# Kernel tuning notes

Hardware: AMD Instinct MI355X
Metric: run time of the kernel (lower is better)

Reference implementation:

```python
import jax, jax.numpy as jnp
import numpy as np

N_NODES = 50000
N_EDGES = 800000
IN_DIM = 128
HIDDEN = 32
NHEAD = 4
OUT_DIM = 64
NEG_SLOPE = 0.2


def setup_inputs() -> dict:
    key = jax.random.key(0)
    ks = jax.random.split(key, 8)
    x = jax.random.normal(ks[0], (N_NODES, IN_DIM), dtype=jnp.float32)
    edge_index = jax.random.randint(ks[1], (2, N_EDGES), 0, N_NODES, dtype=jnp.int64)
    # layer 1: fc (in_dim -> nhead*hidden), attn [nhead, 2*hidden]
    W1 = jax.random.normal(ks[2], (IN_DIM, NHEAD * HIDDEN), dtype=jnp.float32) * 0.1
    attn1 = jax.random.normal(ks[3], (NHEAD, 2 * HIDDEN), dtype=jnp.float32) * 0.1
    # layer 2: fc (nhead*hidden -> 1*out_dim), attn [1, 2*out_dim]
    W2 = jax.random.normal(ks[4], (NHEAD * HIDDEN, OUT_DIM), dtype=jnp.float32) * 0.1
    attn2 = jax.random.normal(ks[5], (1, 2 * OUT_DIM), dtype=jnp.float32) * 0.1
    # extra output head: Linear(out_dim, out_dim) with bias
    head_W = jax.random.normal(ks[6], (OUT_DIM, OUT_DIM), dtype=jnp.float32) * 0.1
    head_b = jax.random.normal(ks[7], (OUT_DIM,), dtype=jnp.float32) * 0.1
    return {"x": x, "edge_index": edge_index, "W1": W1, "attn1": attn1,
            "W2": W2, "attn2": attn2, "head_W": head_W, "head_b": head_b}


def _gat_layer(x, W, attn, row, col, num_nodes, heads):
    """One GATConv: linear proj, edge attention, segment softmax over dst (col), scatter-add."""
    f_out = W.shape[1] // heads
    h = (x @ W).reshape(num_nodes, heads, f_out)            # [N, H, F]
    a_l, a_r = attn[:, :f_out], attn[:, f_out:]              # split attn for src/dst parts
    e_src = jnp.einsum('nhf,hf->nh', h, a_l)                 # [N, H]
    e_dst = jnp.einsum('nhf,hf->nh', h, a_r)                 # [N, H]
    alpha = e_src[row] + e_dst[col]                          # [E, H] == cat(h[row],h[col])·attn
    alpha = jax.nn.leaky_relu(alpha, NEG_SLOPE)
    # segment softmax grouped by destination node (col); self-loops guarantee non-empty segs
    amax = jax.ops.segment_max(alpha, col, num_segments=num_nodes)
    ex = jnp.exp(alpha - amax[col])
    denom = jax.ops.segment_sum(ex, col, num_segments=num_nodes)
    a = ex / denom[col]                                      # [E, H]
    msg = h[row] * a[:, :, None]                             # [E, H, F]
    out = jax.ops.segment_sum(msg, col, num_segments=num_nodes)  # [N, H, F]
    return out.reshape(num_nodes, heads * f_out)


def reference(x, edge_index, W1, attn1, W2, attn2, head_W, head_b):
    n = x.shape[0]
    loops = jnp.arange(n, dtype=edge_index.dtype)
    row = jnp.concatenate([edge_index[0], loops])
    col = jnp.concatenate([edge_index[1], loops])
    h = _gat_layer(x, W1, attn1, row, col, n, NHEAD)         # [N, NHEAD*HIDDEN]
    h = jax.nn.relu(h)                                       # intermediate-layer activation
    h = _gat_layer(h, W2, attn2, row, col, n, 1)             # [N, OUT_DIM] (last: no act)
    out = h @ head_W + head_b                                # extra_output_fc head
    return out
```

## Files before the change

kernel.cpp:

```cpp
#include <hip/hip_runtime.h>
#include <math.h>

#define N_NODES 50000
#define E_RAW 800000
#define E_TOT 850000
#define NEG_SLOPE 0.2f
#define G1_BLOCKS ((N_NODES + 63) / 64)
#define NBUCK 391
#define EPB 2048
#define PBLK ((E_TOT + EPB - 1) / EPB)

typedef __attribute__((ext_vector_type(8))) short bf16x8;
typedef __attribute__((ext_vector_type(4))) float f32x4;

__device__ __forceinline__ float lrelu(float a) { return a > 0.f ? a : NEG_SLOPE * a; }

__device__ __forceinline__ unsigned f2bf(float f) {
    unsigned u = __float_as_uint(f);
    return (u + 0x7fff + ((u >> 16) & 1)) >> 16;
}
__device__ __forceinline__ unsigned pack2(float a, float b) {
    return f2bf(a) | (f2bf(b) << 16);
}
__device__ __forceinline__ float bflo(unsigned p) { return __uint_as_float(p << 16); }
__device__ __forceinline__ float bfhi(unsigned p) { return __uint_as_float(p & 0xffff0000u); }

__global__ void k_prep(const float* __restrict__ W1, const float* __restrict__ W2,
                       unsigned* __restrict__ Btg, unsigned* __restrict__ B2tg) {
    int c = blockIdx.x;
    int tq = threadIdx.x;
    if (c < 128) {
        Btg[c * 64 + tq] = pack2(W1[(2 * tq) * 128 + c], W1[(2 * tq + 1) * 128 + c]);
    } else {
        int c2 = c - 128;
        B2tg[c2 * 64 + tq] = pack2(W2[(2 * tq) * 64 + c2], W2[(2 * tq + 1) * 64 + c2]);
    }
}

__global__ void k_gemm1_p1(const float* __restrict__ A, const unsigned* __restrict__ Btg,
                           const float* __restrict__ aux, uint2* __restrict__ C,
                           float* __restrict__ es, float* __restrict__ ed,
                           const int* __restrict__ ei, int* __restrict__ hist2d) {
    __shared__ unsigned As[64 * 64];
    if (blockIdx.x >= G1_BLOCKS) {
        int blk = blockIdx.x - G1_BLOCKS;
        int* h = (int*)As;
        for (int i = threadIdx.x; i < NBUCK; i += 256) h[i] = 0;
        __syncthreads();
        int base = blk * EPB;
        for (int i = threadIdx.x; i < EPB; i += 256) {
            int e = base + i;
            if (e >= E_TOT) break;
            int col = (e < E_RAW) ? ei[E_RAW + e] : (e - E_RAW);
            atomicAdd(&h[col >> 7], 1);
        }
        __syncthreads();
        for (int i = threadIdx.x; i < NBUCK; i += 256) hist2d[i * PBLK + blk] = h[i];
        return;
    }
    int t = threadIdx.x;
    int m0 = blockIdx.x * 64;
    int rows = min(64, N_NODES - m0);
    const float4* A4 = (const float4*)(A + (size_t)m0 * 128);
    for (int i = t; i < rows * 32; i += 256) {
        int row = i >> 5, k4 = i & 31;
        float4 v = A4[i];
        int byte = (k4 * 8) ^ ((row & 7) << 4);
        unsigned* p = &As[row * 64 + (byte >> 2)];
        p[0] = pack2(v.x, v.y);
        p[1] = pack2(v.z, v.w);
    }
    __syncthreads();
    int lane = t & 63, wave = t >> 6;
    int r15 = lane & 15, g = lane >> 4;
    int arow = wave * 16 + r15;
    f32x4 acc[8];
#pragma unroll
    for (int i = 0; i < 8; ++i) acc[i] = (f32x4){0.f, 0.f, 0.f, 0.f};
    const char* Abase = (const char*)As + arow * 256;
    int swz = (arow & 7) << 4;
    const char* Bbase = (const char*)Btg;
#pragma unroll
    for (int s = 0; s < 4; ++s) {
        bf16x8 xf = *(const bf16x8*)(Abase + ((64 * s + 16 * g) ^ swz));
#pragma unroll
        for (int tt = 0; tt < 8; ++tt) {
            bf16x8 wf = *(const bf16x8*)(Bbase + ((16 * tt + r15) * 256 + 64 * s + 16 * g));
            acc[tt] = __builtin_amdgcn_mfma_f32_16x16x32_bf16(wf, xf, acc[tt], 0, 0, 0);
        }
    }
    int grow = m0 + arow;
    bool valid = (arow < rows);
    if (valid) {
        uint2* C2 = C + (size_t)grow * 32;
#pragma unroll
        for (int tt = 0; tt < 8; ++tt) {
            uint2 v; v.x = pack2(acc[tt][0], acc[tt][1]); v.y = pack2(acc[tt][2], acc[tt][3]);
            C2[4 * tt + g] = v;
        }
    }
    float ps0 = 0.f, ps1 = 0.f, ps2 = 0.f, ps3 = 0.f;
    float pd0 = 0.f, pd1 = 0.f, pd2 = 0.f, pd3 = 0.f;
#pragma unroll
    for (int tt = 0; tt < 8; ++tt) {
        int h = tt >> 1;
        int fin = 16 * (tt & 1) + 4 * g;
        float4 alv = *(const float4*)(aux + h * 64 + fin);
        float4 arv = *(const float4*)(aux + h * 64 + 32 + fin);
        float s4 = acc[tt][0] * alv.x + acc[tt][1] * alv.y + acc[tt][2] * alv.z + acc[tt][3] * alv.w;
        float d4 = acc[tt][0] * arv.x + acc[tt][1] * arv.y + acc[tt][2] * arv.z + acc[tt][3] * arv.w;
        if (h == 0) { ps0 += s4; pd0 += d4; }
        else if (h == 1) { ps1 += s4; pd1 += d4; }
        else if (h == 2) { ps2 += s4; pd2 += d4; }
        else { ps3 += s4; pd3 += d4; }
    }
#pragma unroll
    for (int mask = 16; mask <= 32; mask <<= 1) {
        ps0 += __shfl_xor(ps0, mask); ps1 += __shfl_xor(ps1, mask);
        ps2 += __shfl_xor(ps2, mask); ps3 += __shfl_xor(ps3, mask);
        pd0 += __shfl_xor(pd0, mask); pd1 += __shfl_xor(pd1, mask);
        pd2 += __shfl_xor(pd2, mask); pd3 += __shfl_xor(pd3, mask);
    }
    if (valid) {
        float psg = (g == 0) ? ps0 : (g == 1) ? ps1 : (g == 2) ? ps2 : ps3;
        float pdg = (g == 0) ? pd0 : (g == 1) ? pd1 : (g == 2) ? pd2 : pd3;
        es[grow * 4 + g] = psg;
        ed[grow * 4 + g] = pdg;
    }
}

__global__ void k_p2a(const int* __restrict__ hist2d, int* __restrict__ off2d,
                      int* __restrict__ bucktot) {
    __shared__ int sh[512];
    int b = blockIdx.x, t = threadIdx.x;
    int v = (t < PBLK) ? hist2d[b * PBLK + t] : 0;
    sh[t] = v;
    __syncthreads();
    for (int ofs = 1; ofs < 512; ofs <<= 1) {
        int u = (t >= ofs) ? sh[t - ofs] : 0;
        __syncthreads();
        sh[t] += u;
        __syncthreads();
    }
    if (t < PBLK) off2d[b * PBLK + t] = sh[t] - v;
    if (t == 511) bucktot[b] = sh[511];
}

__global__ void k_p2b(const int* __restrict__ bucktot, int* __restrict__ bucketbase) {
    __shared__ int sh[512];
    int t = threadIdx.x;
    int v = (t < NBUCK) ? bucktot[t] : 0;
    sh[t] = v;
    __syncthreads();
    for (int ofs = 1; ofs < 512; ofs <<= 1) {
        int u = (t >= ofs) ? sh[t - ofs] : 0;
        __syncthreads();
        sh[t] += u;
        __syncthreads();
    }
    if (t < NBUCK) bucketbase[t] = sh[t] - v;
    if (t == 511) bucketbase[NBUCK] = sh[511];
}

__global__ void k_p3(const int* __restrict__ ei, const int* __restrict__ off2d,
                     const int* __restrict__ bucketbase, unsigned* __restrict__ part) {
    __shared__ int h[NBUCK];
    __shared__ int basebuf[NBUCK];
    int blk = blockIdx.x, t = threadIdx.x;
    for (int i = t; i < NBUCK; i += 256) {
        h[i] = 0;
        basebuf[i] = bucketbase[i] + off2d[i * PBLK + blk];
    }
    __syncthreads();
    int base = blk * EPB;
    for (int i = t; i < EPB; i += 256) {
        int e = base + i;
        if (e >= E_TOT) break;
        int col, src;
        if (e < E_RAW) { col = ei[E_RAW + e]; src = ei[e]; }
        else { col = src = e - E_RAW; }
        int b = col >> 7;
        int lr = atomicAdd(&h[b], 1);
        part[basebuf[b] + lr] = (unsigned)src | ((unsigned)(col & 127) << 16);
    }
}

__global__ void k_p4(const unsigned* __restrict__ part, const int* __restrict__ bucketbase,
                     int* __restrict__ off, unsigned short* __restrict__ srcs) {
    __shared__ int h[128];
    __shared__ int colofs[128];
    int b = blockIdx.x, t = threadIdx.x;
    int s0 = bucketbase[b], s1 = bucketbase[b + 1];
    if (t < 128) h[t] = 0;
    __syncthreads();
    for (int i = s0 + t; i < s1; i += 256) atomicAdd(&h[part[i] >> 16], 1);
    __syncthreads();
    if (t == 0) {
        int acc = 0;
        for (int c = 0; c < 128; ++c) { colofs[c] = acc; acc += h[c]; }
    }
    __syncthreads();
    int colbase = b * 128, ncols = min(128, N_NODES - colbase);
    if (t < ncols) off[colbase + t] = s0 + colofs[t];
    if (b == NBUCK - 1 && t == 0) off[N_NODES] = s1;
    if (t < 128) h[t] = colofs[t];
    __syncthreads();
    for (int i = s0 + t; i < s1; i += 256) {
        unsigned u = part[i];
        int c = u >> 16;
        int slot = atomicAdd(&h[c], 1);
        srcs[s0 + slot] = (unsigned short)(u & 0xffffu);
    }
}

__global__ void k_gemm2m(const unsigned* __restrict__ A, const unsigned* __restrict__ B2tg,
                         const float* __restrict__ aux, uint2* __restrict__ C,
                         float* __restrict__ es, float* __restrict__ ed) {
    __shared__ unsigned As[64 * 64];
    int t = threadIdx.x;
    int m0 = blockIdx.x * 64;
    int rows = min(64, N_NODES - m0);
    const uint4* A4 = (const uint4*)(A + (size_t)m0 * 64);
    for (int i = t; i < rows * 16; i += 256) {
        int row = i >> 4, q = i & 15;
        uint4 v = A4[i];
        int byte = (q * 16) ^ ((row & 7) << 4);
        unsigned* p = &As[row * 64 + (byte >> 2)];
        p[0] = v.x; p[1] = v.y; p[2] = v.z; p[3] = v.w;
    }
    __syncthreads();
    int lane = t & 63, wave = t >> 6;
    int r15 = lane & 15, g = lane >> 4;
    int arow = wave * 16 + r15;
    f32x4 acc[4];
#pragma unroll
    for (int i = 0; i < 4; ++i) acc[i] = (f32x4){0.f, 0.f, 0.f, 0.f};
    const char* Abase = (const char*)As + arow * 256;
    int swz = (arow & 7) << 4;
    const char* Bbase = (const char*)B2tg;
#pragma unroll
    for (int s = 0; s < 4; ++s) {
        bf16x8 xf = *(const bf16x8*)(Abase + ((64 * s + 16 * g) ^ swz));
#pragma unroll
        for (int tt = 0; tt < 4; ++tt) {
            bf16x8 wf = *(const bf16x8*)(Bbase + ((16 * tt + r15) * 256 + 64 * s + 16 * g));
            acc[tt] = __builtin_amdgcn_mfma_f32_16x16x32_bf16(wf, xf, acc[tt], 0, 0, 0);
        }
    }
    int grow = m0 + arow;
    bool valid = (arow < rows);
    if (valid) {
        uint2* C2 = C + (size_t)grow * 16;
#pragma unroll
        for (int tt = 0; tt < 4; ++tt) {
            uint2 v; v.x = pack2(acc[tt][0], acc[tt][1]); v.y = pack2(acc[tt][2], acc[tt][3]);
            C2[4 * tt + g] = v;
        }
    }
    float pl = 0.f, pr = 0.f;
#pragma unroll
    for (int tt = 0; tt < 4; ++tt) {
        int f0 = 16 * tt + 4 * g;
        float4 alv = *(const float4*)(aux + f0);
        float4 arv = *(const float4*)(aux + 64 + f0);
        pl += acc[tt][0] * alv.x + acc[tt][1] * alv.y + acc[tt][2] * alv.z + acc[tt][3] * alv.w;
        pr += acc[tt][0] * arv.x + acc[tt][1] * arv.y + acc[tt][2] * arv.z + acc[tt][3] * arv.w;
    }
#pragma unroll
    for (int mask = 16; mask <= 32; mask <<= 1) {
        pl += __shfl_xor(pl, mask);
        pr += __shfl_xor(pr, mask);
    }
    if (valid && g == 0) { es[grow] = pl; ed[grow] = pr; }
}

__global__ void k_head(const float* __restrict__ A, const float* __restrict__ B,
                       const float* __restrict__ aux, float* __restrict__ Cv) {
    constexpr int K = 64, MT = 32;
    __shared__ float As[MT * K];
    int m0 = blockIdx.x * MT;
    int t = threadIdx.x, g = t >> 4, l = t & 15;
    int rows = min(MT, N_NODES - m0);
    const float4* A4 = (const float4*)(A + (size_t)m0 * K);
    float4* S4 = (float4*)As;
    for (int i = t; i < rows * (K / 4); i += 64) S4[i] = A4[i];
    __syncthreads();
    float acc[8][4];
#pragma unroll
    for (int r = 0; r < 8; ++r)
#pragma unroll
        for (int c = 0; c < 4; ++c) acc[r][c] = 0.f;
    const float4* B4 = (const float4*)B;
    for (int kk = 0; kk < K / 4; ++kk) {
        float4 b0 = B4[(4 * kk + 0) * 16 + l];
        float4 b1 = B4[(4 * kk + 1) * 16 + l];
        float4 b2 = B4[(4 * kk + 2) * 16 + l];
        float4 b3 = B4[(4 * kk + 3) * 16 + l];
#pragma unroll
        for (int r = 0; r < 8; ++r) {
            float4 a = ((const float4*)(As + (g * 8 + r) * K))[kk];
            acc[r][0] = fmaf(a.x, b0.x, fmaf(a.y, b1.x, fmaf(a.z, b2.x, fmaf(a.w, b3.x, acc[r][0]))));
            acc[r][1] = fmaf(a.x, b0.y, fmaf(a.y, b1.y, fmaf(a.z, b2.y, fmaf(a.w, b3.y, acc[r][1]))));
            acc[r][2] = fmaf(a.x, b0.z, fmaf(a.y, b1.z, fmaf(a.z, b2.z, fmaf(a.w, b3.z, acc[r][2]))));
            acc[r][3] = fmaf(a.x, b0.w, fmaf(a.y, b1.w, fmaf(a.z, b2.w, fmaf(a.w, b3.w, acc[r][3]))));
        }
    }
    float4* C = (float4*)Cv;
    float4 bv = ((const float4*)aux)[l];
#pragma unroll
    for (int r = 0; r < 8; ++r) {
        int row = m0 + g * 8 + r;
        if (row < N_NODES) {
            float4 v;
            v.x = acc[r][0] + bv.x; v.y = acc[r][1] + bv.y;
            v.z = acc[r][2] + bv.z; v.w = acc[r][3] + bv.w;
            C[(size_t)row * 16 + l] = v;
        }
    }
}

__global__ void k_agg1(const unsigned* __restrict__ h1b, const float* __restrict__ es,
                       const float* __restrict__ ed, const int* __restrict__ off,
                       const unsigned short* __restrict__ srcs, unsigned* __restrict__ out1) {
    int n = blockIdx.x * (blockDim.x >> 6) + (threadIdx.x >> 6);
    int lane = threadIdx.x & 63;
    if (n >= N_NODES) return;
    int myh = lane & 3;
    int jj = lane >> 2;
    float edh = ed[n * 4 + myh];
    int s = off[n], e = off[n + 1];
    int l16 = lane & 15;
    int esub = lane >> 4;
    int hcL = l16 >> 2;
    float acc[8];
#pragma unroll
    for (int i = 0; i < 8; ++i) acc[i] = 0.f;
    float psum = 0.f;
    for (int base = s; base < e; base += 16) {
        int cnt = e - base;
        int srcj = 0;
        float w = 0.f;
        if (jj < cnt) {
            srcj = srcs[base + jj];
            w = __expf(lrelu(es[srcj * 4 + myh] + edh));
        }
        psum += w;
        for (int j2 = 0; j2 < 16 && j2 < cnt; j2 += 4) {
            int eidx = j2 + esub;
            int src = __shfl(srcj, eidx * 4);
            float wv = __shfl(w, eidx * 4 + hcL);
            uint4 pv = *((const uint4*)(h1b + (size_t)src * 64 + l16 * 4));
            acc[0] = fmaf(bflo(pv.x), wv, acc[0]);
            acc[1] = fmaf(bfhi(pv.x), wv, acc[1]);
            acc[2] = fmaf(bflo(pv.y), wv, acc[2]);
            acc[3] = fmaf(bfhi(pv.y), wv, acc[3]);
            acc[4] = fmaf(bflo(pv.z), wv, acc[4]);
            acc[5] = fmaf(bfhi(pv.z), wv, acc[5]);
            acc[6] = fmaf(bflo(pv.w), wv, acc[6]);
            acc[7] = fmaf(bfhi(pv.w), wv, acc[7]);
        }
    }
#pragma unroll
    for (int mask = 4; mask <= 32; mask <<= 1) psum += __shfl_xor(psum, mask);
    float inv = 1.f / __shfl(psum, hcL);
#pragma unroll
    for (int i = 0; i < 8; ++i) {
        acc[i] += __shfl_xor(acc[i], 16);
        acc[i] += __shfl_xor(acc[i], 32);
    }
    if (esub == 0) {
        uint4 o;
        o.x = pack2(fmaxf(acc[0] * inv, 0.f), fmaxf(acc[1] * inv, 0.f));
        o.y = pack2(fmaxf(acc[2] * inv, 0.f), fmaxf(acc[3] * inv, 0.f));
        o.z = pack2(fmaxf(acc[4] * inv, 0.f), fmaxf(acc[5] * inv, 0.f));
        o.w = pack2(fmaxf(acc[6] * inv, 0.f), fmaxf(acc[7] * inv, 0.f));
        *((uint4*)(out1 + (size_t)n * 64 + l16 * 4)) = o;
    }
}

__global__ void k_agg2(const unsigned* __restrict__ h2b, const float* __restrict__ es,
                       const float* __restrict__ ed, const int* __restrict__ off,
                       const unsigned short* __restrict__ srcs, float* __restrict__ outv) {
    int n = blockIdx.x * (blockDim.x >> 6) + (threadIdx.x >> 6);
    int lane = threadIdx.x & 63;
    if (n >= N_NODES) return;
    float edv = ed[n];
    int s = off[n], e = off[n + 1];
    int l16 = lane & 15;
    int esub = lane >> 4;
    const uint2* gp = (const uint2*)h2b;
    float a0 = 0.f, a1 = 0.f, a2 = 0.f, a3 = 0.f, psum = 0.f;
    for (int base = s; base < e; base += 16) {
        int cnt = e - base;
        int srcj = 0;
        float w = 0.f;
        if (lane < 16 && lane < cnt) {
            srcj = srcs[base + lane];
            w = __expf(lrelu(es[srcj] + edv));
        }
        psum += w;
        for (int j2 = 0; j2 < 16 && j2 < cnt; j2 += 4) {
            int eidx = j2 + esub;
            int src = __shfl(srcj, eidx);
            float wv = __shfl(w, eidx);
            uint2 pv = gp[(size_t)src * 16 + l16];
            a0 = fmaf(bflo(pv.x), wv, a0);
            a1 = fmaf(bfhi(pv.x), wv, a1);
            a2 = fmaf(bflo(pv.y), wv, a2);
            a3 = fmaf(bfhi(pv.y), wv, a3);
        }
    }
#pragma unroll
    for (int mask = 1; mask <= 8; mask <<= 1) psum += __shfl_xor(psum, mask);
    float inv = 1.f / __shfl(psum, 0);
    a0 += __shfl_xor(a0, 16); a0 += __shfl_xor(a0, 32);
    a1 += __shfl_xor(a1, 16); a1 += __shfl_xor(a1, 32);
    a2 += __shfl_xor(a2, 16); a2 += __shfl_xor(a2, 32);
    a3 += __shfl_xor(a3, 16); a3 += __shfl_xor(a3, 32);
    if (esub == 0) {
        float4 o;
        o.x = a0 * inv; o.y = a1 * inv; o.z = a2 * inv; o.w = a3 * inv;
        ((float4*)outv)[(size_t)n * 16 + l16] = o;
    }
}

extern "C" void kernel_launch(void* const* d_in, const int* in_sizes, int n_in,
                              void* d_out, int out_size, void* d_ws, size_t ws_size,
                              hipStream_t stream) {
    const float* x     = (const float*)d_in[0];
    const int*   ei    = (const int*)d_in[1];
    const float* W1    = (const float*)d_in[2];
    const float* attn1 = (const float*)d_in[3];
    const float* W2    = (const float*)d_in[4];
    const float* attn2 = (const float*)d_in[5];
    const float* headW = (const float*)d_in[6];
    const float* headb = (const float*)d_in[7];
    float* out = (float*)d_out;

    char* ws = (char*)d_ws;
    size_t o = 0;
    auto alloc = [&](size_t bytes) -> void* {
        o = (o + 255) & ~(size_t)255;
        void* p = ws + o;
        o += bytes;
        return p;
    };
    unsigned*       h1b    = (unsigned*)alloc((size_t)N_NODES * 128 * 2);
    unsigned*       out1b  = (unsigned*)alloc((size_t)N_NODES * 128 * 2);
    unsigned*       h2b    = (unsigned*)alloc((size_t)N_NODES * 64 * 2);
    float*          h2agg  = (float*)alloc((size_t)N_NODES * 64 * 4);
    float*          e1s    = (float*)alloc((size_t)N_NODES * 4 * 4);
    float*          e1d    = (float*)alloc((size_t)N_NODES * 4 * 4);
    float*          e2s    = (float*)alloc((size_t)N_NODES * 4);
    float*          e2d    = (float*)alloc((size_t)N_NODES * 4);
    int*            off    = (int*)alloc((size_t)(N_NODES + 1) * 4);
    unsigned short* srcs   = (unsigned short*)alloc((size_t)E_TOT * 2);
    unsigned*       Btg    = (unsigned*)alloc((size_t)128 * 64 * 4);
    unsigned*       B2tg   = (unsigned*)alloc((size_t)64 * 64 * 4);
    int*            hist2d = (int*)alloc((size_t)NBUCK * PBLK * 4);
    int*            off2d  = (int*)alloc((size_t)NBUCK * PBLK * 4);
    int*            bucktot = (int*)alloc((size_t)NBUCK * 4);
    int*            bucketbase = (int*)alloc((size_t)(NBUCK + 1) * 4);
    unsigned*       part   = (unsigned*)alloc((size_t)E_TOT * 4);

    k_prep<<<192, 64, 0, stream>>>(W1, W2, Btg, B2tg);

    k_gemm1_p1<<<G1_BLOCKS + PBLK, 256, 0, stream>>>(
        x, Btg, attn1, (uint2*)h1b, e1s, e1d, ei, hist2d);

    k_p2a<<<NBUCK, 512, 0, stream>>>(hist2d, off2d, bucktot);
    k_p2b<<<1, 512, 0, stream>>>(bucktot, bucketbase);
    k_p3<<<PBLK, 256, 0, stream>>>(ei, off2d, bucketbase, part);
    k_p4<<<NBUCK, 256, 0, stream>>>(part, bucketbase, off, srcs);

    k_agg1<<<N_NODES / 4, 256, 0, stream>>>(h1b, e1s, e1d, off, srcs, out1b);

    k_gemm2m<<<(N_NODES + 63) / 64, 256, 0, stream>>>(out1b, B2tg, attn2, (uint2*)h2b, e2s, e2d);
    k_agg2<<<N_NODES / 4, 256, 0, stream>>>(h2b, e2s, e2d, off, srcs, h2agg);

    k_head<<<(N_NODES + 31) / 32, 64, 0, stream>>>(h2agg, headW, headb, out);
}
```

Baseline: 229.8 us.

## Fold bucket scan into partition kernels, fuse head into agg2, batch gather loads

Removes the single-block bucket-base scan kernel by having each partition block recompute the prefix scan of bucket totals redundantly, which also raises those kernels to 512 threads. Fuses the output linear head into the layer-2 aggregation kernel, staging head weights in shared memory so the fp32 intermediate is never written to or re-read from global memory. Restructures both aggregation inner loops to issue four gather loads before consuming them, increasing memory-level parallelism. The trade-offs are redundant scan work per block, a 16KB weight load per aggregation block, and removal of the early-exit and the partial-edge-group guard in the gather loops.

After: 219.5 us. 4.5% less time.

```diff
diff --git a/kernel.cpp b/kernel.cpp
--- a/kernel.cpp
+++ b/kernel.cpp
@@ -146,34 +146,26 @@
     if (t == 511) bucktot[b] = sh[511];
 }
 
-__global__ void k_p2b(const int* __restrict__ bucktot, int* __restrict__ bucketbase) {
+__global__ void k_p3(const int* __restrict__ ei, const int* __restrict__ off2d,
+                     const int* __restrict__ bucktot, unsigned* __restrict__ part) {
     __shared__ int sh[512];
-    int t = threadIdx.x;
-    int v = (t < NBUCK) ? bucktot[t] : 0;
-    sh[t] = v;
-    __syncthreads();
-    for (int ofs = 1; ofs < 512; ofs <<= 1) {
-        int u = (t >= ofs) ? sh[t - ofs] : 0;
-        __syncthreads();
-        sh[t] += u;
-        __syncthreads();
-    }
-    if (t < NBUCK) bucketbase[t] = sh[t] - v;
-    if (t == 511) bucketbase[NBUCK] = sh[511];
-}
-
-__global__ void k_p3(const int* __restrict__ ei, const int* __restrict__ off2d,
-                     const int* __restrict__ bucketbase, unsigned* __restrict__ part) {
     __shared__ int h[NBUCK];
     __shared__ int basebuf[NBUCK];
     int blk = blockIdx.x, t = threadIdx.x;
-    for (int i = t; i < NBUCK; i += 256) {
-        h[i] = 0;
-        basebuf[i] = bucketbase[i] + off2d[i * PBLK + blk];
-    }
+    int v = (t < NBUCK) ? bucktot[t] : 0;
+    sh[t] = v;
+    if (t < NBUCK) h[t] = 0;
+    __syncthreads();
+    for (int ofs = 1; ofs < 512; ofs <<= 1) {
+        int u = (t >= ofs) ? sh[t - ofs] : 0;
+        __syncthreads();
+        sh[t] += u;
+        __syncthreads();
+    }
+    if (t < NBUCK) basebuf[t] = (sh[t] - v) + off2d[t * PBLK + blk];
     __syncthreads();
     int base = blk * EPB;
-    for (int i = t; i < EPB; i += 256) {
+    for (int i = t; i < EPB; i += 512) {
         int e = base + i;
         if (e >= E_TOT) break;
         int col, src;
@@ -185,15 +177,27 @@
     }
 }
 
-__global__ void k_p4(const unsigned* __restrict__ part, const int* __restrict__ bucketbase,
+__global__ void k_p4(const unsigned* __restrict__ part, const int* __restrict__ bucktot,
                      int* __restrict__ off, unsigned short* __restrict__ srcs) {
+    __shared__ int sh[512];
     __shared__ int h[128];
     __shared__ int colofs[128];
+    __shared__ int s0sh, s1sh;
     int b = blockIdx.x, t = threadIdx.x;
-    int s0 = bucketbase[b], s1 = bucketbase[b + 1];
+    int v = (t < NBUCK) ? bucktot[t] : 0;
+    sh[t] = v;
     if (t < 128) h[t] = 0;
     __syncthreads();
-    for (int i = s0 + t; i < s1; i += 256) atomicAdd(&h[part[i] >> 16], 1);
+    for (int ofs = 1; ofs < 512; ofs <<= 1) {
+        int u = (t >= ofs) ? sh[t - ofs] : 0;
+        __syncthreads();
+        sh[t] += u;
+        __syncthreads();
+    }
+    if (t == 0) { s1sh = sh[b]; s0sh = sh[b] - bucktot[b]; }
+    __syncthreads();
+    int s0 = s0sh, s1 = s1sh;
+    for (int i = s0 + t; i < s1; i += 512) atomicAdd(&h[part[i] >> 16], 1);
     __syncthreads();
     if (t == 0) {
         int acc = 0;
@@ -205,7 +209,7 @@
     if (b == NBUCK - 1 && t == 0) off[N_NODES] = s1;
     if (t < 128) h[t] = colofs[t];
     __syncthreads();
-    for (int i = s0 + t; i < s1; i += 256) {
+    for (int i = s0 + t; i < s1; i += 512) {
         unsigned u = part[i];
         int c = u >> 16;
         int slot = atomicAdd(&h[c], 1);
@@ -274,51 +278,6 @@
     if (valid && g == 0) { es[grow] = pl; ed[grow] = pr; }
 }
 
-__global__ void k_head(const float* __restrict__ A, const float* __restrict__ B,
-                       const float* __restrict__ aux, float* __restrict__ Cv) {
-    constexpr int K = 64, MT = 32;
-    __shared__ float As[MT * K];
-    int m0 = blockIdx.x * MT;
-    int t = threadIdx.x, g = t >> 4, l = t & 15;
-    int rows = min(MT, N_NODES - m0);
-    const float4* A4 = (const float4*)(A + (size_t)m0 * K);
-    float4* S4 = (float4*)As;
-    for (int i = t; i < rows * (K / 4); i += 64) S4[i] = A4[i];
-    __syncthreads();
-    float acc[8][4];
-#pragma unroll
-    for (int r = 0; r < 8; ++r)
-#pragma unroll
-        for (int c = 0; c < 4; ++c) acc[r][c] = 0.f;
-    const float4* B4 = (const float4*)B;
-    for (int kk = 0; kk < K / 4; ++kk) {
-        float4 b0 = B4[(4 * kk + 0) * 16 + l];
-        float4 b1 = B4[(4 * kk + 1) * 16 + l];
-        float4 b2 = B4[(4 * kk + 2) * 16 + l];
-        float4 b3 = B4[(4 * kk + 3) * 16 + l];
-#pragma unroll
-        for (int r = 0; r < 8; ++r) {
-            float4 a = ((const float4*)(As + (g * 8 + r) * K))[kk];
-            acc[r][0] = fmaf(a.x, b0.x, fmaf(a.y, b1.x, fmaf(a.z, b2.x, fmaf(a.w, b3.x, acc[r][0]))));
-            acc[r][1] = fmaf(a.x, b0.y, fmaf(a.y, b1.y, fmaf(a.z, b2.y, fmaf(a.w, b3.y, acc[r][1]))));
-            acc[r][2] = fmaf(a.x, b0.z, fmaf(a.y, b1.z, fmaf(a.z, b2.z, fmaf(a.w, b3.z, acc[r][2]))));
-            acc[r][3] = fmaf(a.x, b0.w, fmaf(a.y, b1.w, fmaf(a.z, b2.w, fmaf(a.w, b3.w, acc[r][3]))));
-        }
-    }
-    float4* C = (float4*)Cv;
-    float4 bv = ((const float4*)aux)[l];
-#pragma unroll
-    for (int r = 0; r < 8; ++r) {
-        int row = m0 + g * 8 + r;
-        if (row < N_NODES) {
-            float4 v;
-            v.x = acc[r][0] + bv.x; v.y = acc[r][1] + bv.y;
-            v.z = acc[r][2] + bv.z; v.w = acc[r][3] + bv.w;
-            C[(size_t)row * 16 + l] = v;
-        }
-    }
-}
-
 __global__ void k_agg1(const unsigned* __restrict__ h1b, const float* __restrict__ es,
                        const float* __restrict__ ed, const int* __restrict__ off,
                        const unsigned short* __restrict__ srcs, unsigned* __restrict__ out1) {
@@ -345,19 +304,29 @@
             w = __expf(lrelu(es[srcj * 4 + myh] + edh));
         }
         psum += w;
-        for (int j2 = 0; j2 < 16 && j2 < cnt; j2 += 4) {
-            int eidx = j2 + esub;
-            int src = __shfl(srcj, eidx * 4);
-            float wv = __shfl(w, eidx * 4 + hcL);
-            uint4 pv = *((const uint4*)(h1b + (size_t)src * 64 + l16 * 4));
-            acc[0] = fmaf(bflo(pv.x), wv, acc[0]);
-            acc[1] = fmaf(bfhi(pv.x), wv, acc[1]);
-            acc[2] = fmaf(bflo(pv.y), wv, acc[2]);
-            acc[3] = fmaf(bfhi(pv.y), wv, acc[3]);
-            acc[4] = fmaf(bflo(pv.z), wv, acc[4]);
-            acc[5] = fmaf(bfhi(pv.z), wv, acc[5]);
-            acc[6] = fmaf(bflo(pv.w), wv, acc[6]);
-            acc[7] = fmaf(bfhi(pv.w), wv, acc[7]);
+        int src4[4];
+        float wv4[4];
+#pragma unroll
+        for (int q = 0; q < 4; ++q) {
+            int eidx = 4 * q + esub;
+            src4[q] = __shfl(srcj, eidx * 4);
+            wv4[q] = __shfl(w, eidx * 4 + hcL);
+        }
+        uint4 pv4[4];
+#pragma unroll
+        for (int q = 0; q < 4; ++q)
+            pv4[q] = *((const uint4*)(h1b + (size_t)src4[q] * 64 + l16 * 4));
+#pragma unroll
+        for (int q = 0; q < 4; ++q) {
+            float wv = wv4[q];
+            acc[0] = fmaf(bflo(pv4[q].x), wv, acc[0]);
+            acc[1] = fmaf(bfhi(pv4[q].x), wv, acc[1]);
+            acc[2] = fmaf(bflo(pv4[q].y), wv, acc[2]);
+            acc[3] = fmaf(bfhi(pv4[q].y), wv, acc[3]);
+            acc[4] = fmaf(bflo(pv4[q].z), wv, acc[4]);
+            acc[5] = fmaf(bfhi(pv4[q].z), wv, acc[5]);
+            acc[6] = fmaf(bflo(pv4[q].w), wv, acc[6]);
+            acc[7] = fmaf(bfhi(pv4[q].w), wv, acc[7]);
         }
     }
 #pragma unroll
@@ -378,12 +347,22 @@
     }
 }
 
-__global__ void k_agg2(const unsigned* __restrict__ h2b, const float* __restrict__ es,
-                       const float* __restrict__ ed, const int* __restrict__ off,
-                       const unsigned short* __restrict__ srcs, float* __restrict__ outv) {
-    int n = blockIdx.x * (blockDim.x >> 6) + (threadIdx.x >> 6);
-    int lane = threadIdx.x & 63;
-    if (n >= N_NODES) return;
+__global__ void k_agg2h(const unsigned* __restrict__ h2b, const float* __restrict__ es,
+                        const float* __restrict__ ed, const int* __restrict__ off,
+                        const unsigned short* __restrict__ srcs,
+                        const float* __restrict__ headW, const float* __restrict__ headb,
+                        float* __restrict__ outv) {
+    __shared__ float Wsh[64 * 64];
+    __shared__ float rowsh[4][64];
+    int t = threadIdx.x;
+    {
+        const float4* W4 = (const float4*)headW;
+        float4* S4 = (float4*)Wsh;
+        for (int i = t; i < 1024; i += 256) S4[i] = W4[i];
+    }
+    int wavei = t >> 6;
+    int n = blockIdx.x * 4 + wavei;
+    int lane = t & 63;
     float edv = ed[n];
     int s = off[n], e = off[n + 1];
     int l16 = lane & 15;
@@ -399,15 +378,23 @@
             w = __expf(lrelu(es[srcj] + edv));
         }
         psum += w;
-        for (int j2 = 0; j2 < 16 && j2 < cnt; j2 += 4) {
-            int eidx = j2 + esub;
-            int src = __shfl(srcj, eidx);
-            float wv = __shfl(w, eidx);
-            uint2 pv = gp[(size_t)src * 16 + l16];
-            a0 = fmaf(bflo(pv.x), wv, a0);
-            a1 = fmaf(bfhi(pv.x), wv, a1);
-            a2 = fmaf(bflo(pv.y), wv, a2);
-            a3 = fmaf(bfhi(pv.y), wv, a3);
+        int src4[4];
+        float wv4[4];
+#pragma unroll
+        for (int q = 0; q < 4; ++q) {
+            int eidx = 4 * q + esub;
+            src4[q] = __shfl(srcj, eidx);
+            wv4[q] = __shfl(w, eidx);
+        }
+        uint2 pv4[4];
+#pragma unroll
+        for (int q = 0; q < 4; ++q) pv4[q] = gp[(size_t)src4[q] * 16 + l16];
+#pragma unroll
+        for (int q = 0; q < 4; ++q) {
+            a0 = fmaf(bflo(pv4[q].x), wv4[q], a0);
+            a1 = fmaf(bfhi(pv4[q].x), wv4[q], a1);
+            a2 = fmaf(bflo(pv4[q].y), wv4[q], a2);
+            a3 = fmaf(bfhi(pv4[q].y), wv4[q], a3);
         }
     }
 #pragma unroll
@@ -418,10 +405,17 @@
     a2 += __shfl_xor(a2, 16); a2 += __shfl_xor(a2, 32);
     a3 += __shfl_xor(a3, 16); a3 += __shfl_xor(a3, 32);
     if (esub == 0) {
-        float4 o;
-        o.x = a0 * inv; o.y = a1 * inv; o.z = a2 * inv; o.w = a3 * inv;
-        ((float4*)outv)[(size_t)n * 16 + l16] = o;
-    }
+        rowsh[wavei][4 * l16 + 0] = a0 * inv;
+        rowsh[wavei][4 * l16 + 1] = a1 * inv;
+        rowsh[wavei][4 * l16 + 2] = a2 * inv;
+        rowsh[wavei][4 * l16 + 3] = a3 * inv;
+    }
+    __syncthreads();
+    float hacc = headb[lane];
+#pragma unroll 8
+    for (int k = 0; k < 64; ++k)
+        hacc = fmaf(rowsh[wavei][k], Wsh[k * 64 + lane], hacc);
+    outv[(size_t)n * 64 + lane] = hacc;
 }
 
 extern "C" void kernel_launch(void* const* d_in, const int* in_sizes, int n_in,
@@ -448,7 +442,6 @@
     unsigned*       h1b    = (unsigned*)alloc((size_t)N_NODES * 128 * 2);
     unsigned*       out1b  = (unsigned*)alloc((size_t)N_NODES * 128 * 2);
     unsigned*       h2b    = (unsigned*)alloc((size_t)N_NODES * 64 * 2);
-    float*          h2agg  = (float*)alloc((size_t)N_NODES * 64 * 4);
     float*          e1s    = (float*)alloc((size_t)N_NODES * 4 * 4);
     float*          e1d    = (float*)alloc((size_t)N_NODES * 4 * 4);
     float*          e2s    = (float*)alloc((size_t)N_NODES * 4);
@@ -460,7 +453,6 @@
     int*            hist2d = (int*)alloc((size_t)NBUCK * PBLK * 4);
     int*            off2d  = (int*)alloc((size_t)NBUCK * PBLK * 4);
     int*            bucktot = (int*)alloc((size_t)NBUCK * 4);
-    int*            bucketbase = (int*)alloc((size_t)(NBUCK + 1) * 4);
     unsigned*       part   = (unsigned*)alloc((size_t)E_TOT * 4);
 
     k_prep<<<192, 64, 0, stream>>>(W1, W2, Btg, B2tg);
@@ -469,14 +461,11 @@
         x, Btg, attn1, (uint2*)h1b, e1s, e1d, ei, hist2d);
 
     k_p2a<<<NBUCK, 512, 0, stream>>>(hist2d, off2d, bucktot);
-    k_p2b<<<1, 512, 0, stream>>>(bucktot, bucketbase);
-    k_p3<<<PBLK, 256, 0, stream>>>(ei, off2d, bucketbase, part);
-    k_p4<<<NBUCK, 256, 0, stream>>>(part, bucketbase, off, srcs);
+    k_p3<<<PBLK, 512, 0, stream>>>(ei, off2d, bucktot, part);
+    k_p4<<<NBUCK, 512, 0, stream>>>(part, bucktot, off, srcs);
 
     k_agg1<<<N_NODES / 4, 256, 0, stream>>>(h1b, e1s, e1d, off, srcs, out1b);
 
     k_gemm2m<<<(N_NODES + 63) / 64, 256, 0, stream>>>(out1b, B2tg, attn2, (uint2*)h2b, e2s, e2d);
-    k_agg2<<<N_NODES / 4, 256, 0, stream>>>(h2b, e2s, e2d, off, srcs, h2agg);
-
-    k_head<<<(N_NODES + 31) / 32, 64, 0, stream>>>(h2agg, headW, headb, out);
-}
+    k_agg2h<<<N_NODES / 4, 256, 0, stream>>>(h2b, e2s, e2d, off, srcs, headW, headb, out);
+}
```
